# Optimization experiments

Hardware: AMD Instinct MI355X
Metric: run time of the kernel (lower is better)

Reference implementation:

```python
import jax, jax.numpy as jnp
import numpy as np
import jax.scipy.signal as jss

SX, SY, C, K = 256, 256, 3, 10
C0 = [0, 0, 0, 1, 1, 1, 2, 2, 2, 0]
C1 = [[0, 1, 2, 9], [3, 4, 5], [6, 7, 8]]
DD, DT, SIGMA = 5, 0.2, 0.65

_KX = jnp.array([[-1., 0., 1.], [-2., 0., 2.], [-1., 0., 1.]])
_KY = _KX.T


def _conv2(A, Kf):
    # zero-padded 'same' 2D true convolution, vmapped over channel axis
    return jax.vmap(lambda a: jss.convolve2d(a, Kf, mode='same'), in_axes=2, out_axes=2)(A)


def sobel(A):
    # (X, Y, c) -> (X, Y, 2, c): [sobel_y, sobel_x] stacked on axis 2 (FlowLenia convention)
    return jnp.concatenate([_conv2(A, _KY)[:, :, None, :], _conv2(A, _KX)[:, :, None, :]], axis=2)


def growth(U, m, s):
    # bell(U,m,s)*2 - 1
    return jnp.exp(-((U - m) / s) ** 2 / 2.) * 2. - 1.


def get_kernels_fft(R, r, a, w, b):
    # FlowLenia kernel construction: ring distance -> smooth cutoff * sum-of-bumps, normalized, fft2(fftshift)
    mid = SX // 2
    xs = jnp.arange(-mid, mid, dtype=jnp.float32)
    D = jnp.sqrt(xs[:, None] ** 2 + xs[None, :] ** 2)            # (X, Y)
    Dk = D[..., None] / ((R + 15.) * r)                          # (X, Y, k)
    ker = (b * jnp.exp(-(Dk[..., None] - a) ** 2 / w)).sum(-1)   # (X, Y, k)
    sig = 0.5 * (jnp.tanh(-(Dk - 1.) * 10. / 2.) + 1.)           # sigmoid(-(D-1)*10)
    Kk = sig * ker
    nK = Kk / Kk.sum(axis=(0, 1), keepdims=True)
    return jnp.fft.fft2(jnp.fft.fftshift(nK, axes=(0, 1)), axes=(0, 1))


def _rt_apply(A, F):
    # Reintegration tracking with 'wall' border: flow-driven mass redistribution over a (2dd+1)^2 neighborhood
    ii = jnp.arange(SX, dtype=jnp.float32)
    pos = jnp.stack(jnp.meshgrid(ii, ii, indexing='ij'), axis=-1) + 0.5   # (X, Y, 2) cell centers
    ma = DD - SIGMA                                   # max flow magnitude
    mu = pos[..., None] + jnp.clip(DT * F, -ma, ma)   # (X, Y, 2, C) target centers
    mu = jnp.clip(mu, SIGMA, SX - SIGMA)              # wall border
    offs = jnp.arange(-DD, DD + 1)
    gx, gy = jnp.meshgrid(offs, offs, indexing='ij')
    dxs, dys = gx.reshape(-1), gy.reshape(-1)
    clip_hi = min(1., 2. * SIGMA)

    def step(dx, dy):
        Ar = jnp.roll(A, (dx, dy), axis=(0, 1))
        mur = jnp.roll(mu, (dx, dy), axis=(0, 1))
        dpmu = jnp.abs(pos[..., None] - mur)                                  # (X, Y, 2, C)
        sz = 0.5 - dpmu + SIGMA
        area = jnp.prod(jnp.clip(sz, 0., clip_hi), axis=2) / (4. * SIGMA ** 2)  # (X, Y, C)
        return Ar * area

    return jax.vmap(step)(dxs, dys).sum(axis=0)


def setup_inputs() -> dict:
    key = jax.random.key(0)
    ks = jax.random.split(key, 9)
    A = jax.random.uniform(ks[0], (SX, SY, C), dtype=jnp.float32)
    R = jax.random.uniform(ks[1], (), minval=2.0, maxval=25.0)
    r = jax.random.uniform(ks[2], (K,), minval=0.2, maxval=1.0)
    m = jax.random.uniform(ks[3], (K,), minval=0.05, maxval=0.5)
    s = jax.random.uniform(ks[4], (K,), minval=0.001, maxval=0.18)
    h = jax.random.uniform(ks[5], (K,), minval=0.01, maxval=1.0)
    a = jax.random.uniform(ks[6], (K, 3), minval=0.0, maxval=1.0)
    b = jax.random.uniform(ks[7], (K, 3), minval=0.001, maxval=1.0)
    w = jax.random.uniform(ks[8], (K, 3), minval=0.01, maxval=0.5)
    return dict(A=A, R=R, r=r, m=m, s=s, h=h, a=a, b=b, w=w)


def reference(A, R, r, m, s, h, a, b, w):
    fK = get_kernels_fft(R, r, a, w, b)                       # (X, Y, k) complex
    fA = jnp.fft.fft2(A, axes=(0, 1))
    fAk = fA[:, :, jnp.array(C0)]                             # (X, Y, k)
    U = jnp.real(jnp.fft.ifft2(fK * fAk, axes=(0, 1)))        # (X, Y, k)
    U = growth(U, m, s) * h
    U = jnp.dstack([U[:, :, C1[c]].sum(axis=-1) for c in range(C)])  # (X, Y, C)
    nabla_U = sobel(U)                                        # (X, Y, 2, C)
    nabla_A = sobel(A.sum(axis=-1, keepdims=True))            # (X, Y, 2, 1)
    alpha = jnp.clip((A[:, :, None, :] / C) ** 2, 0., 1.)     # (X, Y, 1, C)
    F = nabla_U * (1. - alpha) - nabla_A * alpha              # (X, Y, 2, C)
    return _rt_apply(A, F)
```

## Files before the change

kernel.cpp:

```cpp
#include <hip/hip_runtime.h>

#define NPIX 65536

#define WS_APLANE 0
#define WS_ASUM   (3*NPIX)
#define WS_KOFF   (4*NPIX)
#define WS_MUX    (4*NPIX)
#define WS_MUY    (7*NPIX)
#define WS_UACC   (14*NPIX)
#define WS_ROWS   (24*NPIX)
#define WS_X1RE   (25*NPIX)
#define WS_X1IM   (38*NPIX)
#define WS_X2RE   (51*NPIX)
#define WS_X2IM   (64*NPIX)
#define WS_END    (77*NPIX)

__global__ void k_prep(const float* __restrict__ A,
                       const float* __restrict__ R_, const float* __restrict__ r_,
                       const float* __restrict__ a_, const float* __restrict__ b_,
                       const float* __restrict__ w_, float* __restrict__ ws) {
    int bid = blockIdx.x;
    int t = threadIdx.x;
    if (bid < 256) {
        int idx = bid * 256 + t;
        float a0 = A[idx*3+0], a1 = A[idx*3+1], a2 = A[idx*3+2];
        ws[WS_APLANE + idx]          = a0;
        ws[WS_APLANE + NPIX + idx]   = a1;
        ws[WS_APLANE + 2*NPIX + idx] = a2;
        ws[WS_ASUM + idx] = a0 + a1 + a2;
        return;
    }
    __shared__ float red[4];
    int bk = bid - 256;
    int k = bk >> 8;
    int i = bk & 255;
    int wid = t >> 6, lane = t & 63;
    float R = R_[0];
    float denom = (R + 15.0f) * r_[k];
    int di = i - 128, dj = t - 128;
    float D  = sqrtf((float)(di*di + dj*dj));
    float Dk = D / denom;
    float v = 0.0f;
    if (Dk <= 3.0f) {
        float ker = 0.0f;
        #pragma unroll
        for (int tt = 0; tt < 3; ++tt) {
            float d = Dk - a_[k*3+tt];
            ker += b_[k*3+tt] * expf(-((d*d) / w_[k*3+tt]));
        }
        float sig = 1.0f / (1.0f + expf(10.0f * (Dk - 1.0f)));
        v = sig * ker;
    }
    int iw = (i + 128) & 255;
    int jw = (t + 128) & 255;
    ws[WS_KOFF + k*NPIX + iw*256 + jw] = v;
    float s = v;
    #pragma unroll
    for (int off = 32; off; off >>= 1) s += __shfl_xor(s, off);
    if (lane == 0) red[wid] = s;
    __syncthreads();
    if (t == 0) ws[WS_ROWS + k*256 + i] = red[0] + red[1] + red[2] + red[3];
}

__device__ __forceinline__ void fft256_core(float* __restrict__ re, float* __restrict__ im,
                                            const float* __restrict__ twr,
                                            const float* __restrict__ twi, int lane) {
    #pragma unroll
    for (int s = 1; s <= 8; ++s) {
        int h = 1 << (s - 1);
        #pragma unroll
        for (int b = 0; b < 2; ++b) {
            int idx = b*64 + lane;
            int pos = idx & (h - 1);
            int g   = idx >> (s - 1);
            int i0 = (g << s) + pos;
            int i1 = i0 + h;
            int tj = pos << (8 - s);
            float wr = twr[tj], wi = twi[tj];
            float xr = re[i1], xi = im[i1];
            float br = fmaf(xr, wr, -xi*wi);
            float bi = fmaf(xr, wi,  xi*wr);
            float ar = re[i0], ai = im[i0];
            re[i0] = ar + br; im[i0] = ai + bi;
            re[i1] = ar - br; im[i1] = ai - bi;
        }
    }
}

__device__ __forceinline__ void build_tw(float* twr, float* twi, int t, float sgn) {
    if (t < 128) {
        float ang = (float)t * 0.0245436930f;
        twr[t] = cosf(ang);
        twi[t] = sgn * sinf(ang);
    }
}

__device__ __forceinline__ void store_t4(float* __restrict__ dst, const float* __restrict__ buf,
                                         int off, int t, int lb) {
    float4 v;
    v.x = buf[0*512 + off + t];
    v.y = buf[1*512 + off + t];
    v.z = buf[2*512 + off + t];
    v.w = buf[3*512 + off + t];
    *(float4*)&dst[t*256 + lb] = v;
}

__global__ __launch_bounds__(256) void fft_fwd_packed(float* __restrict__ ws) {
    __shared__ float buf[4*512];
    __shared__ float twr[128], twi[128];
    int p  = blockIdx.x >> 6;
    int lb = (blockIdx.x & 63) * 4;
    int wid = threadIdx.x >> 6, lane = threadIdx.x & 63;
    int t = threadIdx.x;
    build_tw(twr, twi, t, -1.0f);
    int f = 2*p, g = 2*p + 1;
    const float* frow = ws + ((f < 3) ? (WS_APLANE + f*NPIX) : (WS_KOFF + (f-3)*NPIX))
                      + (lb + wid)*256;
    const float* grow = (g < 13)
        ? ws + ((g < 3) ? (WS_APLANE + g*NPIX) : (WS_KOFF + (g-3)*NPIX)) + (lb + wid)*256
        : nullptr;
    float* re = &buf[wid*512];
    float* im = re + 256;
    #pragma unroll
    for (int e = 0; e < 4; ++e) {
        int idx = e*64 + lane;
        int dst = __brev(idx) >> 24;
        re[dst] = frow[idx];
        im[dst] = grow ? grow[idx] : 0.0f;
    }
    __syncthreads();
    fft256_core(re, im, twr, twi, lane);
    __syncthreads();
    int u2 = (256 - t) & 255;
    float4 Fre, Fim, Gre, Gim;
    float* pF[4] = {&Fre.x, &Fim.x, &Gre.x, &Gim.x};
    #pragma unroll
    for (int l = 0; l < 4; ++l) {
        float zr1 = buf[l*512 + t],  zi1 = buf[l*512 + 256 + t];
        float zr2 = buf[l*512 + u2], zi2 = buf[l*512 + 256 + u2];
        pF[0][l] = 0.5f*(zr1 + zr2);
        pF[1][l] = 0.5f*(zi1 - zi2);
        pF[2][l] = 0.5f*(zi1 + zi2);
        pF[3][l] = 0.5f*(zr2 - zr1);
    }
    *(float4*)&ws[WS_X1RE + f*NPIX + t*256 + lb] = Fre;
    *(float4*)&ws[WS_X1IM + f*NPIX + t*256 + lb] = Fim;
    if (g < 13) {
        *(float4*)&ws[WS_X1RE + g*NPIX + t*256 + lb] = Gre;
        *(float4*)&ws[WS_X1IM + g*NPIX + t*256 + lb] = Gim;
    }
}

__global__ __launch_bounds__(256) void fft_fwd_cplx(float* __restrict__ ws) {
    __shared__ float buf[4*512];
    __shared__ float twr[128], twi[128];
    int p  = blockIdx.x >> 6;
    int lb = (blockIdx.x & 63) * 4;
    int wid = threadIdx.x >> 6, lane = threadIdx.x & 63;
    int t = threadIdx.x;
    build_tw(twr, twi, t, -1.0f);
    float* re = &buf[wid*512];
    float* im = re + 256;
    const float* rr = ws + WS_X1RE + p*NPIX + (lb + wid)*256;
    const float* ri = ws + WS_X1IM + p*NPIX + (lb + wid)*256;
    #pragma unroll
    for (int e = 0; e < 4; ++e) {
        int idx = e*64 + lane;
        int dst = __brev(idx) >> 24;
        re[dst] = rr[idx];
        im[dst] = ri[idx];
    }
    __syncthreads();
    fft256_core(re, im, twr, twi, lane);
    __syncthreads();
    store_t4(ws + WS_X2RE + p*NPIX, buf, 0,   t, lb);
    store_t4(ws + WS_X2IM + p*NPIX, buf, 256, t, lb);
}

__global__ __launch_bounds__(256) void ifft_mul_packed(float* __restrict__ ws) {
    __shared__ float buf[4*512];
    __shared__ float twr[128], twi[128];
    int j  = blockIdx.x >> 6;
    int lb = (blockIdx.x & 63) * 4;
    int wid = threadIdx.x >> 6, lane = threadIdx.x & 63;
    int t = threadIdx.x;
    build_tw(twr, twi, t, 1.0f);
    const int C0[10] = {0,0,0,1,1,1,2,2,2,0};
    int ka = 2*j, kb = 2*j + 1;
    int ca = C0[ka], cb = C0[kb];
    int rowoff = (lb + wid)*256;
    const float* arp = ws + WS_X2RE + ca*NPIX + rowoff;
    const float* aip = ws + WS_X2IM + ca*NPIX + rowoff;
    const float* krp = ws + WS_X2RE + (3+ka)*NPIX + rowoff;
    const float* kip = ws + WS_X2IM + (3+ka)*NPIX + rowoff;
    const float* brp = ws + WS_X2RE + cb*NPIX + rowoff;
    const float* bip = ws + WS_X2IM + cb*NPIX + rowoff;
    const float* lrp = ws + WS_X2RE + (3+kb)*NPIX + rowoff;
    const float* lip = ws + WS_X2IM + (3+kb)*NPIX + rowoff;
    float* re = &buf[wid*512];
    float* im = re + 256;
    #pragma unroll
    for (int e = 0; e < 4; ++e) {
        int idx = e*64 + lane;
        int dst = __brev(idx) >> 24;
        float ar = arp[idx], ai = aip[idx];
        float kr = krp[idx], ki = kip[idx];
        float uar = ar*kr - ai*ki;
        float uai = ar*ki + ai*kr;
        float br = brp[idx], bi = bip[idx];
        float lr = lrp[idx], li = lip[idx];
        float ubr = br*lr - bi*li;
        float ubi = br*li + bi*lr;
        re[dst] = uar - ubi;
        im[dst] = uai + ubr;
    }
    __syncthreads();
    fft256_core(re, im, twr, twi, lane);
    __syncthreads();
    store_t4(ws + WS_X1RE + j*NPIX, buf, 0,   t, lb);
    store_t4(ws + WS_X1IM + j*NPIX, buf, 256, t, lb);
}

__global__ __launch_bounds__(256) void ifft_real_packed(float* __restrict__ ws) {
    __shared__ float buf[4*512];
    __shared__ float twr[128], twi[128];
    int j  = blockIdx.x >> 6;
    int lb = (blockIdx.x & 63) * 4;
    int wid = threadIdx.x >> 6, lane = threadIdx.x & 63;
    int t = threadIdx.x;
    build_tw(twr, twi, t, 1.0f);
    float* re = &buf[wid*512];
    float* im = re + 256;
    const float* rr = ws + WS_X1RE + j*NPIX + (lb + wid)*256;
    const float* ri = ws + WS_X1IM + j*NPIX + (lb + wid)*256;
    #pragma unroll
    for (int e = 0; e < 4; ++e) {
        int idx = e*64 + lane;
        int dst = __brev(idx) >> 24;
        re[dst] = rr[idx];
        im[dst] = ri[idx];
    }
    __syncthreads();
    fft256_core(re, im, twr, twi, lane);
    __syncthreads();
    const float sc = 1.0f / 65536.0f;
    float4 va, vb;
    va.x = buf[0*512 + t] * sc;       vb.x = buf[0*512 + 256 + t] * sc;
    va.y = buf[1*512 + t] * sc;       vb.y = buf[1*512 + 256 + t] * sc;
    va.z = buf[2*512 + t] * sc;       vb.z = buf[2*512 + 256 + t] * sc;
    va.w = buf[3*512 + t] * sc;       vb.w = buf[3*512 + 256 + t] * sc;
    *(float4*)&ws[WS_UACC + (2*j)*NPIX   + t*256 + lb] = va;
    *(float4*)&ws[WS_UACC + (2*j+1)*NPIX + t*256 + lb] = vb;
}

__device__ inline void sobel_at(const float* __restrict__ p, int x, int y,
                                float& gy, float& gx) {
    float v[3][3];
    #pragma unroll
    for (int ii = -1; ii <= 1; ++ii)
        #pragma unroll
        for (int jj = -1; jj <= 1; ++jj) {
            int xx = x + ii, yy = y + jj;
            v[ii+1][jj+1] = (xx < 0 || xx > 255 || yy < 0 || yy > 255)
                            ? 0.0f : p[xx*256 + yy];
        }
    gy = (v[0][0] + 2.0f*v[0][1] + v[0][2]) - (v[2][0] + 2.0f*v[2][1] + v[2][2]);
    gx = (v[0][0] + 2.0f*v[1][0] + v[2][0]) - (v[0][2] + 2.0f*v[1][2] + v[2][2]);
}

__global__ __launch_bounds__(256) void growth_mu(float* __restrict__ ws,
                                                 const float* __restrict__ m_,
                                                 const float* __restrict__ s_,
                                                 const float* __restrict__ h_) {
    __shared__ float Ush[3][256];
    __shared__ float kinv[4];
    int b = blockIdx.x;
    int c = b >> 8;
    int x = b & 255;
    int t = threadIdx.x, wid = t >> 6, lane = t & 63;
    int nk = (c == 0) ? 4 : 3;
    if (wid < nk) {
        int k = (wid == 3) ? 9 : c*3 + wid;
        const float* rw = ws + WS_ROWS + k*256;
        float v = rw[lane] + rw[64+lane] + rw[128+lane] + rw[192+lane];
        #pragma unroll
        for (int off = 32; off; off >>= 1) v += __shfl_xor(v, off);
        if (lane == 0) kinv[wid] = 1.0f / v;
    }
    __syncthreads();
    const float* uacc = ws + WS_UACC;
    for (int rr = 0; rr < 3; ++rr) {
        int xr = x - 1 + rr;
        float outv = 0.0f;
        if (xr >= 0 && xr <= 255) {
            int idx = xr*256 + t;
            for (int kk = 0; kk < nk; ++kk) {
                int k = (kk == 3) ? 9 : c*3 + kk;
                float U = uacc[k*NPIX + idx] * kinv[kk];
                float z = (U - m_[k]) / s_[k];
                outv += h_[k] * (expf(-0.5f*z*z)*2.0f - 1.0f);
            }
        }
        Ush[rr][t] = outv;
    }
    __syncthreads();
    int y = t;
    float gyA, gxA;
    sobel_at(ws + WS_ASUM, x, y, gyA, gxA);
    float v[3][3];
    #pragma unroll
    for (int ii = -1; ii <= 1; ++ii)
        #pragma unroll
        for (int jj = -1; jj <= 1; ++jj) {
            int xx = x + ii, yy = y + jj;
            v[ii+1][jj+1] = (xx < 0 || xx > 255 || yy < 0 || yy > 255)
                            ? 0.0f : Ush[ii+1][yy];
        }
    float gy = (v[0][0] + 2.0f*v[0][1] + v[0][2]) - (v[2][0] + 2.0f*v[2][1] + v[2][2]);
    float gx = (v[0][0] + 2.0f*v[1][0] + v[2][0]) - (v[0][2] + 2.0f*v[1][2] + v[2][2]);
    float a = ws[WS_APLANE + c*NPIX + x*256 + y];
    float al = (a / 3.0f); al = al * al;
    al = fminf(fmaxf(al, 0.0f), 1.0f);
    float F0 = gy * (1.0f - al) - gyA * al;
    float F1 = gx * (1.0f - al) - gxA * al;
    float d0 = fminf(fmaxf(0.2f * F0, -4.35f), 4.35f);
    float d1 = fminf(fmaxf(0.2f * F1, -4.35f), 4.35f);
    ws[WS_MUX + c*NPIX + x*256 + y] = fminf(fmaxf((float)x + 0.5f + d0, 0.65f), 255.35f);
    ws[WS_MUY + c*NPIX + x*256 + y] = fminf(fmaxf((float)y + 0.5f + d1, 0.65f), 255.35f);
}

__global__ __launch_bounds__(256) void rt_apply_v2(const float* __restrict__ ws,
                                                   float* __restrict__ out) {
    __shared__ float sA[11*256], sX[11*256], sY[11*256];
    int b = blockIdx.x;
    int c = b >> 8;
    int x = b & 255;
    const float* ap = ws + WS_APLANE + c*NPIX;
    const float* mx = ws + WS_MUX + c*NPIX;
    const float* my = ws + WS_MUY + c*NPIX;
    int t = threadIdx.x;
    #pragma unroll
    for (int i = 0; i < 11; ++i) {
        int src = (((x - (i - 5)) & 255) << 8) + t;
        sA[i*256 + t] = ap[src];
        sX[i*256 + t] = mx[src];
        sY[i*256 + t] = my[src];
    }
    __syncthreads();
    int y = t;
    float px = (float)x + 0.5f, py = (float)y + 0.5f;
    float acc = 0.0f;
    #pragma unroll
    for (int dx = -5; dx <= 5; ++dx) {
        int rb = (dx + 5) * 256;
        for (int dy = -5; dy <= 5; ++dy) {
            int sy = (y - dy) & 255;
            float a  = sA[rb + sy];
            float ax = 1.15f - fabsf(px - sX[rb + sy]);
            float ay = 1.15f - fabsf(py - sY[rb + sy]);
            ax = fminf(fmaxf(ax, 0.0f), 1.0f);
            ay = fminf(fmaxf(ay, 0.0f), 1.0f);
            acc = fmaf(a, ax * ay, acc);
        }
    }
    out[(x*256 + y)*3 + c] = acc * (1.0f / (4.0f * 0.65f * 0.65f));
}

extern "C" void kernel_launch(void* const* d_in, const int* in_sizes, int n_in,
                              void* d_out, int out_size, void* d_ws, size_t ws_size,
                              hipStream_t stream) {
    const float* A = (const float*)d_in[0];
    const float* R = (const float*)d_in[1];
    const float* r = (const float*)d_in[2];
    const float* m = (const float*)d_in[3];
    const float* s = (const float*)d_in[4];
    const float* h = (const float*)d_in[5];
    const float* a = (const float*)d_in[6];
    const float* b = (const float*)d_in[7];
    const float* w = (const float*)d_in[8];
    float* ws  = (float*)d_ws;
    float* out = (float*)d_out;

    k_prep<<<256 + 2560, 256, 0, stream>>>(A, R, r, a, b, w, ws);
    fft_fwd_packed<<<7*64, 256, 0, stream>>>(ws);
    fft_fwd_cplx<<<13*64, 256, 0, stream>>>(ws);
    ifft_mul_packed<<<5*64, 256, 0, stream>>>(ws);
    ifft_real_packed<<<5*64, 256, 0, stream>>>(ws);
    growth_mu<<<768, 256, 0, stream>>>(ws, m, s, h);
    rt_apply_v2<<<768, 256, 0, stream>>>(ws, out);
}
```

Before: 122.5 us.

## Fuse all pipeline stages into one cooperative persistent kernel with grid syncs

Replaces the seven separate kernel launches with a single cooperative kernel that loops over each stage's work units and separates stages with grid-wide barriers. Shared memory is reused across stages and twiddle tables are built once per direction. The goal is to remove per-launch overhead and inter-kernel gaps. In exchange, occupancy is capped at 512 blocks, grid.sync adds its own cost, and each stage runs fewer concurrent blocks than before. If the cooperative launch fails, the code falls back to separate kernels.

```diff
diff --git a/kernel.cpp b/kernel.cpp
--- a/kernel.cpp
+++ b/kernel.cpp
@@ -1,4 +1,6 @@
 #include <hip/hip_runtime.h>
+#include <hip/hip_cooperative_groups.h>
+namespace cg = cooperative_groups;
 
 #define NPIX 65536
 
@@ -14,53 +16,6 @@
 #define WS_X2RE   (51*NPIX)
 #define WS_X2IM   (64*NPIX)
 #define WS_END    (77*NPIX)
-
-__global__ void k_prep(const float* __restrict__ A,
-                       const float* __restrict__ R_, const float* __restrict__ r_,
-                       const float* __restrict__ a_, const float* __restrict__ b_,
-                       const float* __restrict__ w_, float* __restrict__ ws) {
-    int bid = blockIdx.x;
-    int t = threadIdx.x;
-    if (bid < 256) {
-        int idx = bid * 256 + t;
-        float a0 = A[idx*3+0], a1 = A[idx*3+1], a2 = A[idx*3+2];
-        ws[WS_APLANE + idx]          = a0;
-        ws[WS_APLANE + NPIX + idx]   = a1;
-        ws[WS_APLANE + 2*NPIX + idx] = a2;
-        ws[WS_ASUM + idx] = a0 + a1 + a2;
-        return;
-    }
-    __shared__ float red[4];
-    int bk = bid - 256;
-    int k = bk >> 8;
-    int i = bk & 255;
-    int wid = t >> 6, lane = t & 63;
-    float R = R_[0];
-    float denom = (R + 15.0f) * r_[k];
-    int di = i - 128, dj = t - 128;
-    float D  = sqrtf((float)(di*di + dj*dj));
-    float Dk = D / denom;
-    float v = 0.0f;
-    if (Dk <= 3.0f) {
-        float ker = 0.0f;
-        #pragma unroll
-        for (int tt = 0; tt < 3; ++tt) {
-            float d = Dk - a_[k*3+tt];
-            ker += b_[k*3+tt] * expf(-((d*d) / w_[k*3+tt]));
-        }
-        float sig = 1.0f / (1.0f + expf(10.0f * (Dk - 1.0f)));
-        v = sig * ker;
-    }
-    int iw = (i + 128) & 255;
-    int jw = (t + 128) & 255;
-    ws[WS_KOFF + k*NPIX + iw*256 + jw] = v;
-    float s = v;
-    #pragma unroll
-    for (int off = 32; off; off >>= 1) s += __shfl_xor(s, off);
-    if (lane == 0) red[wid] = s;
-    __syncthreads();
-    if (t == 0) ws[WS_ROWS + k*256 + i] = red[0] + red[1] + red[2] + red[3];
-}
 
 __device__ __forceinline__ void fft256_core(float* __restrict__ re, float* __restrict__ im,
                                             const float* __restrict__ twr,
@@ -87,14 +42,6 @@
     }
 }
 
-__device__ __forceinline__ void build_tw(float* twr, float* twi, int t, float sgn) {
-    if (t < 128) {
-        float ang = (float)t * 0.0245436930f;
-        twr[t] = cosf(ang);
-        twi[t] = sgn * sinf(ang);
-    }
-}
-
 __device__ __forceinline__ void store_t4(float* __restrict__ dst, const float* __restrict__ buf,
                                          int off, int t, int lb) {
     float4 v;
@@ -105,30 +52,82 @@
     *(float4*)&dst[t*256 + lb] = v;
 }
 
-__global__ __launch_bounds__(256) void fft_fwd_packed(float* __restrict__ ws) {
-    __shared__ float buf[4*512];
-    __shared__ float twr[128], twi[128];
-    int p  = blockIdx.x >> 6;
-    int lb = (blockIdx.x & 63) * 4;
-    int wid = threadIdx.x >> 6, lane = threadIdx.x & 63;
-    int t = threadIdx.x;
-    build_tw(twr, twi, t, -1.0f);
+__device__ inline void sobel_at(const float* __restrict__ p, int x, int y,
+                                float& gy, float& gx) {
+    float v[3][3];
+    #pragma unroll
+    for (int ii = -1; ii <= 1; ++ii)
+        #pragma unroll
+        for (int jj = -1; jj <= 1; ++jj) {
+            int xx = x + ii, yy = y + jj;
+            v[ii+1][jj+1] = (xx < 0 || xx > 255 || yy < 0 || yy > 255)
+                            ? 0.0f : p[xx*256 + yy];
+        }
+    gy = (v[0][0] + 2.0f*v[0][1] + v[0][2]) - (v[2][0] + 2.0f*v[2][1] + v[2][2]);
+    gx = (v[0][0] + 2.0f*v[1][0] + v[2][0]) - (v[0][2] + 2.0f*v[1][2] + v[2][2]);
+}
+
+
+__device__ __forceinline__ void body_prep(int u, int t, int wid, int lane,
+    const float* __restrict__ A, float R, const float* __restrict__ r_,
+    const float* __restrict__ a_, const float* __restrict__ b_,
+    const float* __restrict__ w_, float* __restrict__ ws, float* __restrict__ red4) {
+    if (u < 256) {
+        int idx = u*256 + t;
+        float a0 = A[idx*3+0], a1 = A[idx*3+1], a2 = A[idx*3+2];
+        ws[WS_APLANE + idx]          = a0;
+        ws[WS_APLANE + NPIX + idx]   = a1;
+        ws[WS_APLANE + 2*NPIX + idx] = a2;
+        ws[WS_ASUM + idx] = a0 + a1 + a2;
+    } else {
+        int bk = u - 256;
+        int k = bk >> 8, i = bk & 255;
+        float denom = (R + 15.0f) * r_[k];
+        int di = i - 128, dj = t - 128;
+        float D  = sqrtf((float)(di*di + dj*dj));
+        float Dk = D / denom;
+        float v = 0.0f;
+        if (Dk <= 3.0f) {
+            float ker = 0.0f;
+            #pragma unroll
+            for (int tt = 0; tt < 3; ++tt) {
+                float d = Dk - a_[k*3+tt];
+                ker += b_[k*3+tt] * expf(-((d*d) / w_[k*3+tt]));
+            }
+            float sig = 1.0f / (1.0f + expf(10.0f * (Dk - 1.0f)));
+            v = sig * ker;
+        }
+        int iw = (i + 128) & 255, jw = (t + 128) & 255;
+        ws[WS_KOFF + k*NPIX + iw*256 + jw] = v;
+        float ssum = v;
+        #pragma unroll
+        for (int off = 32; off; off >>= 1) ssum += __shfl_xor(ssum, off);
+        __syncthreads();
+        if (lane == 0) red4[wid] = ssum;
+        __syncthreads();
+        if (t == 0) ws[WS_ROWS + k*256 + i] = red4[0]+red4[1]+red4[2]+red4[3];
+    }
+}
+
+__device__ __forceinline__ void body_fft1(int u, int t, int wid, int lane,
+    float* __restrict__ buf, const float* __restrict__ twr, const float* __restrict__ twi,
+    float* __restrict__ ws) {
+    int p = u >> 6, lb = (u & 63) * 4;
     int f = 2*p, g = 2*p + 1;
     const float* frow = ws + ((f < 3) ? (WS_APLANE + f*NPIX) : (WS_KOFF + (f-3)*NPIX))
                       + (lb + wid)*256;
-    const float* grow = (g < 13)
+    const float* grow_ = (g < 13)
         ? ws + ((g < 3) ? (WS_APLANE + g*NPIX) : (WS_KOFF + (g-3)*NPIX)) + (lb + wid)*256
         : nullptr;
-    float* re = &buf[wid*512];
+    float* re = buf + wid*512;
     float* im = re + 256;
     #pragma unroll
     for (int e = 0; e < 4; ++e) {
         int idx = e*64 + lane;
         int dst = __brev(idx) >> 24;
         re[dst] = frow[idx];
-        im[dst] = grow ? grow[idx] : 0.0f;
-    }
-    __syncthreads();
+        im[dst] = grow_ ? grow_[idx] : 0.0f;
+    }
     fft256_core(re, im, twr, twi, lane);
     __syncthreads();
     int u2 = (256 - t) & 255;
@@ -151,15 +150,11 @@
     }
 }
 
-__global__ __launch_bounds__(256) void fft_fwd_cplx(float* __restrict__ ws) {
-    __shared__ float buf[4*512];
-    __shared__ float twr[128], twi[128];
-    int p  = blockIdx.x >> 6;
-    int lb = (blockIdx.x & 63) * 4;
-    int wid = threadIdx.x >> 6, lane = threadIdx.x & 63;
-    int t = threadIdx.x;
-    build_tw(twr, twi, t, -1.0f);
-    float* re = &buf[wid*512];
+__device__ __forceinline__ void body_fft2(int u, int t, int wid, int lane,
+    float* __restrict__ buf, const float* __restrict__ twr, const float* __restrict__ twi,
+    float* __restrict__ ws) {
+    int p = u >> 6, lb = (u & 63) * 4;
+    float* re = buf + wid*512;
     float* im = re + 256;
     const float* rr = ws + WS_X1RE + p*NPIX + (lb + wid)*256;
     const float* ri = ws + WS_X1IM + p*NPIX + (lb + wid)*256;
@@ -170,24 +165,19 @@
         re[dst] = rr[idx];
         im[dst] = ri[idx];
     }
-    __syncthreads();
     fft256_core(re, im, twr, twi, lane);
     __syncthreads();
     store_t4(ws + WS_X2RE + p*NPIX, buf, 0,   t, lb);
     store_t4(ws + WS_X2IM + p*NPIX, buf, 256, t, lb);
 }
 
-__global__ __launch_bounds__(256) void ifft_mul_packed(float* __restrict__ ws) {
-    __shared__ float buf[4*512];
-    __shared__ float twr[128], twi[128];
-    int j  = blockIdx.x >> 6;
-    int lb = (blockIdx.x & 63) * 4;
-    int wid = threadIdx.x >> 6, lane = threadIdx.x & 63;
-    int t = threadIdx.x;
-    build_tw(twr, twi, t, 1.0f);
-    const int C0[10] = {0,0,0,1,1,1,2,2,2,0};
+__device__ __forceinline__ void body_mul(int u, int t, int wid, int lane,
+    float* __restrict__ buf, const float* __restrict__ twr, const float* __restrict__ twi,
+    float* __restrict__ ws) {
+    int j = u >> 6, lb = (u & 63) * 4;
     int ka = 2*j, kb = 2*j + 1;
-    int ca = C0[ka], cb = C0[kb];
+    int ca = (ka < 9) ? ka/3 : 0;
+    int cb = (kb < 9) ? kb/3 : 0;
     int rowoff = (lb + wid)*256;
     const float* arp = ws + WS_X2RE + ca*NPIX + rowoff;
     const float* aip = ws + WS_X2IM + ca*NPIX + rowoff;
@@ -197,7 +187,7 @@
     const float* bip = ws + WS_X2IM + cb*NPIX + rowoff;
     const float* lrp = ws + WS_X2RE + (3+kb)*NPIX + rowoff;
     const float* lip = ws + WS_X2IM + (3+kb)*NPIX + rowoff;
-    float* re = &buf[wid*512];
+    float* re = buf + wid*512;
     float* im = re + 256;
     #pragma unroll
     for (int e = 0; e < 4; ++e) {
@@ -214,22 +204,17 @@
         re[dst] = uar - ubi;
         im[dst] = uai + ubr;
     }
-    __syncthreads();
     fft256_core(re, im, twr, twi, lane);
     __syncthreads();
     store_t4(ws + WS_X1RE + j*NPIX, buf, 0,   t, lb);
     store_t4(ws + WS_X1IM + j*NPIX, buf, 256, t, lb);
 }
 
-__global__ __launch_bounds__(256) void ifft_real_packed(float* __restrict__ ws) {
-    __shared__ float buf[4*512];
-    __shared__ float twr[128], twi[128];
-    int j  = blockIdx.x >> 6;
-    int lb = (blockIdx.x & 63) * 4;
-    int wid = threadIdx.x >> 6, lane = threadIdx.x & 63;
-    int t = threadIdx.x;
-    build_tw(twr, twi, t, 1.0f);
-    float* re = &buf[wid*512];
+__device__ __forceinline__ void body_ifft2(int u, int t, int wid, int lane,
+    float* __restrict__ buf, const float* __restrict__ twr, const float* __restrict__ twi,
+    float* __restrict__ ws) {
+    int j = u >> 6, lb = (u & 63) * 4;
+    float* re = buf + wid*512;
     float* im = re + 256;
     const float* rr = ws + WS_X1RE + j*NPIX + (lb + wid)*256;
     const float* ri = ws + WS_X1IM + j*NPIX + (lb + wid)*256;
@@ -240,44 +225,22 @@
         re[dst] = rr[idx];
         im[dst] = ri[idx];
     }
-    __syncthreads();
     fft256_core(re, im, twr, twi, lane);
     __syncthreads();
     const float sc = 1.0f / 65536.0f;
     float4 va, vb;
-    va.x = buf[0*512 + t] * sc;       vb.x = buf[0*512 + 256 + t] * sc;
-    va.y = buf[1*512 + t] * sc;       vb.y = buf[1*512 + 256 + t] * sc;
-    va.z = buf[2*512 + t] * sc;       vb.z = buf[2*512 + 256 + t] * sc;
-    va.w = buf[3*512 + t] * sc;       vb.w = buf[3*512 + 256 + t] * sc;
+    va.x = buf[0*512 + t] * sc;   vb.x = buf[0*512 + 256 + t] * sc;
+    va.y = buf[1*512 + t] * sc;   vb.y = buf[1*512 + 256 + t] * sc;
+    va.z = buf[2*512 + t] * sc;   vb.z = buf[2*512 + 256 + t] * sc;
+    va.w = buf[3*512 + t] * sc;   vb.w = buf[3*512 + 256 + t] * sc;
     *(float4*)&ws[WS_UACC + (2*j)*NPIX   + t*256 + lb] = va;
     *(float4*)&ws[WS_UACC + (2*j+1)*NPIX + t*256 + lb] = vb;
 }
 
-__device__ inline void sobel_at(const float* __restrict__ p, int x, int y,
-                                float& gy, float& gx) {
-    float v[3][3];
-    #pragma unroll
-    for (int ii = -1; ii <= 1; ++ii)
-        #pragma unroll
-        for (int jj = -1; jj <= 1; ++jj) {
-            int xx = x + ii, yy = y + jj;
-            v[ii+1][jj+1] = (xx < 0 || xx > 255 || yy < 0 || yy > 255)
-                            ? 0.0f : p[xx*256 + yy];
-        }
-    gy = (v[0][0] + 2.0f*v[0][1] + v[0][2]) - (v[2][0] + 2.0f*v[2][1] + v[2][2]);
-    gx = (v[0][0] + 2.0f*v[1][0] + v[2][0]) - (v[0][2] + 2.0f*v[1][2] + v[2][2]);
-}
-
-__global__ __launch_bounds__(256) void growth_mu(float* __restrict__ ws,
-                                                 const float* __restrict__ m_,
-                                                 const float* __restrict__ s_,
-                                                 const float* __restrict__ h_) {
-    __shared__ float Ush[3][256];
-    __shared__ float kinv[4];
-    int b = blockIdx.x;
-    int c = b >> 8;
-    int x = b & 255;
-    int t = threadIdx.x, wid = t >> 6, lane = t & 63;
+__device__ __forceinline__ void body_growth(int u, int t, int wid, int lane,
+    float* __restrict__ Ush, float* __restrict__ kinv, float* __restrict__ ws,
+    const float* __restrict__ m_, const float* __restrict__ s_, const float* __restrict__ h_) {
+    int c = u >> 8, x = u & 255;
     int nk = (c == 0) ? 4 : 3;
     if (wid < nk) {
         int k = (wid == 3) ? 9 : c*3 + wid;
@@ -301,7 +264,7 @@
                 outv += h_[k] * (expf(-0.5f*z*z)*2.0f - 1.0f);
             }
         }
-        Ush[rr][t] = outv;
+        Ush[rr*256 + t] = outv;
     }
     __syncthreads();
     int y = t;
@@ -314,7 +277,7 @@
         for (int jj = -1; jj <= 1; ++jj) {
             int xx = x + ii, yy = y + jj;
             v[ii+1][jj+1] = (xx < 0 || xx > 255 || yy < 0 || yy > 255)
-                            ? 0.0f : Ush[ii+1][yy];
+                            ? 0.0f : Ush[(ii+1)*256 + yy];
         }
     float gy = (v[0][0] + 2.0f*v[0][1] + v[0][2]) - (v[2][0] + 2.0f*v[2][1] + v[2][2]);
     float gx = (v[0][0] + 2.0f*v[1][0] + v[2][0]) - (v[0][2] + 2.0f*v[1][2] + v[2][2]);
@@ -329,16 +292,13 @@
     ws[WS_MUY + c*NPIX + x*256 + y] = fminf(fmaxf((float)y + 0.5f + d1, 0.65f), 255.35f);
 }
 
-__global__ __launch_bounds__(256) void rt_apply_v2(const float* __restrict__ ws,
-                                                   float* __restrict__ out) {
-    __shared__ float sA[11*256], sX[11*256], sY[11*256];
-    int b = blockIdx.x;
-    int c = b >> 8;
-    int x = b & 255;
+__device__ __forceinline__ void body_rt(int u, int t,
+    float* __restrict__ sA, float* __restrict__ sX, float* __restrict__ sY,
+    const float* __restrict__ ws, float* __restrict__ out) {
+    int c = u >> 8, x = u & 255;
     const float* ap = ws + WS_APLANE + c*NPIX;
     const float* mx = ws + WS_MUX + c*NPIX;
     const float* my = ws + WS_MUY + c*NPIX;
-    int t = threadIdx.x;
     #pragma unroll
     for (int i = 0; i < 11; ++i) {
         int src = (((x - (i - 5)) & 255) << 8) + t;
@@ -364,6 +324,119 @@
         }
     }
     out[(x*256 + y)*3 + c] = acc * (1.0f / (4.0f * 0.65f * 0.65f));
+}
+
+__global__ __launch_bounds__(256, 2) void mega(
+    const float* __restrict__ A, const float* __restrict__ R_, const float* __restrict__ r_,
+    const float* __restrict__ m_, const float* __restrict__ s_, const float* __restrict__ h_,
+    const float* __restrict__ a_, const float* __restrict__ b_, const float* __restrict__ w_,
+    float* __restrict__ ws, float* __restrict__ out)
+{
+    __shared__ float smem[8448];
+    cg::grid_group grid = cg::this_grid();
+    const int GB = gridDim.x;
+    int t = threadIdx.x, wid = t >> 6, lane = t & 63;
+
+    float R = R_[0];
+    for (int u = blockIdx.x; u < 2816; u += GB)
+        body_prep(u, t, wid, lane, A, R, r_, a_, b_, w_, ws, smem);
+    grid.sync();
+
+    float* buf = smem;
+    float* twr = smem + 2048;
+    float* twi = smem + 2176;
+    if (t < 128) {
+        float ang = (float)t * 0.0245436930f;
+        twr[t] = cosf(ang); twi[t] = -sinf(ang);
+    }
+    for (int u = blockIdx.x; u < 448; u += GB) {
+        __syncthreads();
+        body_fft1(u, t, wid, lane, buf, twr, twi, ws);
+    }
+    grid.sync();
+    for (int u = blockIdx.x; u < 832; u += GB) {
+        __syncthreads();
+        body_fft2(u, t, wid, lane, buf, twr, twi, ws);
+    }
+    grid.sync();
+    if (t < 128) {
+        float ang = (float)t * 0.0245436930f;
+        twr[t] = cosf(ang); twi[t] = sinf(ang);
+    }
+    for (int u = blockIdx.x; u < 320; u += GB) {
+        __syncthreads();
+        body_mul(u, t, wid, lane, buf, twr, twi, ws);
+    }
+    grid.sync();
+    for (int u = blockIdx.x; u < 320; u += GB) {
+        __syncthreads();
+        body_ifft2(u, t, wid, lane, buf, twr, twi, ws);
+    }
+    grid.sync();
+    for (int u = blockIdx.x; u < 768; u += GB) {
+        __syncthreads();
+        body_growth(u, t, wid, lane, smem, smem + 768, ws, m_, s_, h_);
+    }
+    grid.sync();
+    for (int u = blockIdx.x; u < 768; u += GB) {
+        __syncthreads();
+        body_rt(u, t, smem, smem + 2816, smem + 5632, ws, out);
+    }
+}
+
+__global__ void fb_prep(const float* __restrict__ A, const float* __restrict__ R_,
+                        const float* __restrict__ r_, const float* __restrict__ a_,
+                        const float* __restrict__ b_, const float* __restrict__ w_,
+                        float* __restrict__ ws) {
+    __shared__ float red[4];
+    body_prep(blockIdx.x, threadIdx.x, threadIdx.x >> 6, threadIdx.x & 63,
+              A, R_[0], r_, a_, b_, w_, ws, red);
+}
+__global__ __launch_bounds__(256) void fb_fft1(float* __restrict__ ws) {
+    __shared__ float buf[2048];
+    __shared__ float twr[128], twi[128];
+    int t = threadIdx.x;
+    if (t < 128) { float ang = (float)t * 0.0245436930f; twr[t] = cosf(ang); twi[t] = -sinf(ang); }
+    __syncthreads();
+    body_fft1(blockIdx.x, t, t >> 6, t & 63, buf, twr, twi, ws);
+}
+__global__ __launch_bounds__(256) void fb_fft2(float* __restrict__ ws) {
+    __shared__ float buf[2048];
+    __shared__ float twr[128], twi[128];
+    int t = threadIdx.x;
+    if (t < 128) { float ang = (float)t * 0.0245436930f; twr[t] = cosf(ang); twi[t] = -sinf(ang); }
+    __syncthreads();
+    body_fft2(blockIdx.x, t, t >> 6, t & 63, buf, twr, twi, ws);
+}
+__global__ __launch_bounds__(256) void fb_mul(float* __restrict__ ws) {
+    __shared__ float buf[2048];
+    __shared__ float twr[128], twi[128];
+    int t = threadIdx.x;
+    if (t < 128) { float ang = (float)t * 0.0245436930f; twr[t] = cosf(ang); twi[t] = sinf(ang); }
+    __syncthreads();
+    body_mul(blockIdx.x, t, t >> 6, t & 63, buf, twr, twi, ws);
+}
+__global__ __launch_bounds__(256) void fb_ifft2(float* __restrict__ ws) {
+    __shared__ float buf[2048];
+    __shared__ float twr[128], twi[128];
+    int t = threadIdx.x;
+    if (t < 128) { float ang = (float)t * 0.0245436930f; twr[t] = cosf(ang); twi[t] = sinf(ang); }
+    __syncthreads();
+    body_ifft2(blockIdx.x, t, t >> 6, t & 63, buf, twr, twi, ws);
+}
+__global__ __launch_bounds__(256) void fb_growth(float* __restrict__ ws,
+                                                 const float* __restrict__ m_,
+                                                 const float* __restrict__ s_,
+                                                 const float* __restrict__ h_) {
+    __shared__ float Ush[768];
+    __shared__ float kinv[4];
+    body_growth(blockIdx.x, threadIdx.x, threadIdx.x >> 6, threadIdx.x & 63,
+                Ush, kinv, ws, m_, s_, h_);
+}
+__global__ __launch_bounds__(256) void fb_rt(const float* __restrict__ ws,
+                                             float* __restrict__ out) {
+    __shared__ float sA[2816], sX[2816], sY[2816];
+    body_rt(blockIdx.x, threadIdx.x, sA, sX, sY, ws, out);
 }
 
 extern "C" void kernel_launch(void* const* d_in, const int* in_sizes, int n_in,
@@ -381,11 +454,20 @@
     float* ws  = (float*)d_ws;
     float* out = (float*)d_out;
 
-    k_prep<<<256 + 2560, 256, 0, stream>>>(A, R, r, a, b, w, ws);
-    fft_fwd_packed<<<7*64, 256, 0, stream>>>(ws);
-    fft_fwd_cplx<<<13*64, 256, 0, stream>>>(ws);
-    ifft_mul_packed<<<5*64, 256, 0, stream>>>(ws);
-    ifft_real_packed<<<5*64, 256, 0, stream>>>(ws);
-    growth_mu<<<768, 256, 0, stream>>>(ws, m, s, h);
-    rt_apply_v2<<<768, 256, 0, stream>>>(ws, out);
-}
+    void* args[] = {(void*)&A, (void*)&R, (void*)&r, (void*)&m, (void*)&s, (void*)&h,
+                    (void*)&a, (void*)&b, (void*)&w, (void*)&ws, (void*)&out};
+    hipError_t err = hipLaunchCooperativeKernel((void*)mega, dim3(512), dim3(256),
+                                                args, 0, stream);
+    if (err != hipSuccess)
+        err = hipLaunchCooperativeKernel((void*)mega, dim3(256), dim3(256),
+                                         args, 0, stream);
+    if (err != hipSuccess) {
+        fb_prep<<<2816, 256, 0, stream>>>(A, R, r, a, b, w, ws);
+        fb_fft1<<<448, 256, 0, stream>>>(ws);
+        fb_fft2<<<832, 256, 0, stream>>>(ws);
+        fb_mul<<<320, 256, 0, stream>>>(ws);
+        fb_ifft2<<<320, 256, 0, stream>>>(ws);
+        fb_growth<<<768, 256, 0, stream>>>(ws, m, s, h);
+        fb_rt<<<768, 256, 0, stream>>>(ws, out);
+    }
+}
```

New measurement: 488.1 us. 3.98x slower.
